# Optimization experiments

Measured on AMD Instinct MI355X. Metric: run time of the kernel, lower is better.

Reference implementation:

```python
import jax, jax.numpy as jnp
import numpy as np

J = 24       # num_joints
DIM = 3      # point dim
CD = 128     # c_dim
BN = 4       # bottleneck_size
HPG = 32     # hidden per group (hidden_size=768 / 24)

def setup_inputs() -> dict:
    key = jax.random.key(0)
    ks = jax.random.split(key, 16)
    B, T = 4, 25000
    s = lambda k, shape, fan_in: jax.random.normal(k, shape, jnp.float32) * (1.0 / np.sqrt(fan_in))
    return {
        "p": jax.random.normal(ks[0], (B, J * DIM, T), jnp.float32),
        "z": jax.random.normal(ks[1], (B, 128), jnp.float32),
        "c": jax.random.normal(ks[2], (B, CD), jnp.float32),
        # grouped Conv1d weights stored as (J, out_per_group, in_per_group)
        "W_proj": s(ks[3], (J, BN, CD), CD),          "b_proj": jnp.zeros((J * BN,), jnp.float32),
        "W_p":   s(ks[4], (J, HPG, DIM + BN), DIM+BN), "b_p":   jnp.zeros((J * HPG,), jnp.float32),
        "W0":    s(ks[5], (J, HPG, HPG), HPG),         "b0":    jnp.zeros((J * HPG,), jnp.float32),
        "W1":    s(ks[6], (J, HPG, HPG), HPG),         "b1":    jnp.zeros((J * HPG,), jnp.float32),
        "W2":    s(ks[7], (J, HPG, HPG), HPG),         "b2":    jnp.zeros((J * HPG,), jnp.float32),
        "W_out": s(ks[8], (J, 1, HPG), HPG),           "b_out": jnp.zeros((J,), jnp.float32),
    }

def _gconv(x, W, b):
    # grouped 1x1 conv: x (B,J,Cin,T), W (J,Cout,Cin), b (J*Cout,) -> (B,J,Cout,T)
    y = jnp.einsum('bjit,joi->bjot', x, W)
    return y + b.reshape(1, J, -1, 1)

def reference(p, z, c, W_proj, b_proj, W_p, b_p, W0, b0, W1, b1, W2, b2, W_out, b_out):
    B, _, T = p.shape
    # p.view(B, J, -1, T) then keep last `dim` channels
    p_in = p.reshape(B, J, -1, T)[:, :, -DIM:, :]            # (B,J,3,T)
    # 2D c branch: repeat per joint, grouped proj, broadcast over T
    c_rep = jnp.broadcast_to(c[:, None, :], (B, J, CD))       # (B,J,128)
    c_proj = jnp.einsum('bjc,joc->bjo', c_rep, W_proj) + b_proj.reshape(1, J, BN)
    c_proj = jnp.broadcast_to(c_proj[:, :, :, None], (B, J, BN, T))
    x = jnp.concatenate([p_in, c_proj], axis=2)               # (B,J,3+4,T)
    net = jax.nn.relu(_gconv(x,   W_p, b_p))
    net = jax.nn.relu(_gconv(net, W0,  b0))
    net = jax.nn.relu(_gconv(net, W1,  b1))
    net = jax.nn.relu(_gconv(net, W2,  b2))
    out = _gconv(net, W_out, b_out)                           # (B,J,1,T)
    return out.reshape(B, J, T)                               # logits (B, num_joints, T)
```

## Files before the change

kernel.cpp:

```cpp
#include <hip/hip_runtime.h>
#include <hip/hip_bf16.h>

#define NJ 24
#define TLEN 25000
#define NB 4
#define CHUNKS 10
#define NWPB (CHUNKS*4)
#define NITERS ((TLEN+63)/64)

typedef short short8 __attribute__((ext_vector_type(8)));
typedef short s16x2 __attribute__((ext_vector_type(2)));
typedef float f32x16 __attribute__((ext_vector_type(16)));

union FragU { unsigned u[4]; short8 s; };

__device__ __forceinline__ unsigned pack2(float a, float b){
    unsigned ua = __float_as_uint(a) + 0x8000u;
    unsigned ub = __float_as_uint(b) + 0x8000u;
    return __builtin_amdgcn_perm(ub, ua, 0x07060302u);
}
__device__ __forceinline__ float bflo(unsigned u){
    union { unsigned v; float f; } t; t.v = u << 16; return t.f;
}
__device__ __forceinline__ float bfhi(unsigned u){
    union { unsigned v; float f; } t; t.v = u & 0xffff0000u; return t.f;
}
__device__ __forceinline__ void split2(float a, float b, unsigned &hi, unsigned &lo){
    unsigned hw = pack2(a, b);
    float fa = bflo(hw), fb = bfhi(hw);
    lo = pack2(a - fa, b - fb);
    hi = hw;
}

__device__ __forceinline__ unsigned pkrelu(unsigned x){
    union { unsigned u; s16x2 v; } a, r;
    a.u = x;
    s16x2 z; z[0] = 0; z[1] = 0;
    r.v = __builtin_elementwise_max(a.v, z);
    return r.u;
}

__device__ __forceinline__ f32x16 mfma(const FragU &a, const FragU &b, f32x16 c){
    return __builtin_amdgcn_mfma_f32_32x32x16_bf16(a.s, b.s, c, 0, 0, 0);
}

__device__ __forceinline__ void relu_pack(const f32x16 &acc, FragU &k0, FragU &k1){
    unsigned w[8];
    #pragma unroll
    for (int i = 0; i < 8; ++i) w[i] = pkrelu(pack2(acc[2*i], acc[2*i+1]));
    k0.u[0]=w[0]; k0.u[1]=w[1]; k0.u[2]=w[2]; k0.u[3]=w[3];
    k1.u[0]=w[4]; k1.u[1]=w[5]; k1.u[2]=w[6]; k1.u[3]=w[7];
}

__global__ __launch_bounds__(256, 2) void ptf_decoder_kernel(
    const float* __restrict__ p,    const float* __restrict__ c,
    const float* __restrict__ Wproj,const float* __restrict__ bproj,
    const float* __restrict__ Wp,   const float* __restrict__ bp,
    const float* __restrict__ W0,   const float* __restrict__ b0,
    const float* __restrict__ W1,   const float* __restrict__ b1,
    const float* __restrict__ W2,   const float* __restrict__ b2,
    const float* __restrict__ Wout, const float* __restrict__ bout,
    float* __restrict__ out)
{
    __shared__ __align__(16) float ldsW[3][32][36];
    __shared__ __align__(16) float ldsWp[32][8];
    __shared__ __align__(16) float ldsB[4][32];
    __shared__ __align__(16) float ldsWo[32];

    const int tid = threadIdx.x;
    const int bj  = blockIdx.x % (NB*NJ);
    const int sub = blockIdx.x / (NB*NJ);
    const int b   = bj / NJ;
    const int j   = bj % NJ;

    {
        const float* Wl[3] = {W0, W1, W2};
        #pragma unroll
        for (int L = 0; L < 3; ++L) {
            int row = tid >> 3, c4 = tid & 7;
            float4 v = *reinterpret_cast<const float4*>(Wl[L] + ((size_t)(j*32 + row))*32 + c4*4);
            *reinterpret_cast<float4*>(&ldsW[L][row][c4*4]) = v;
        }
        {
            int row = tid >> 3, i8 = tid & 7;
            ldsWp[row][i8] = (i8 < 7) ? Wp[((size_t)(j*32 + row))*7 + i8] : 0.f;
        }
        if      (tid < 32)  ldsB[0][tid]      = bp[j*32 + tid];
        else if (tid < 64)  ldsB[1][tid-32]   = b0[j*32 + tid-32];
        else if (tid < 96)  ldsB[2][tid-64]   = b1[j*32 + tid-64];
        else if (tid < 128) ldsB[3][tid-96]   = b2[j*32 + tid-96];
        else if (tid < 160) ldsWo[tid-128]    = Wout[j*32 + tid-128];
    }
    __syncthreads();

    const int lane = tid & 63;
    const int row  = lane & 31;
    const int h    = lane >> 5;

    FragU whi[3][2];
    #pragma unroll
    for (int L = 0; L < 3; ++L) {
        #pragma unroll
        for (int kh = 0; kh < 2; ++kh) {
            const int g  = kh*2 + h;
            const int cA = (g >> 1)*4 + (g & 1);
            const float* base = &ldsW[L][row][0];
            float4 x = *reinterpret_cast<const float4*>(base + cA*4);
            float4 y = *reinterpret_cast<const float4*>(base + (cA+2)*4);
            whi[L][kh].u[0] = pack2(x.x, x.y);
            whi[L][kh].u[1] = pack2(x.z, x.w);
            whi[L][kh].u[2] = pack2(y.x, y.y);
            whi[L][kh].u[3] = pack2(y.z, y.w);
        }
    }
    FragU woF[2];
    #pragma unroll
    for (int kh = 0; kh < 2; ++kh) {
        const int g  = kh*2 + h;
        const int cA = (g >> 1)*4 + (g & 1);
        float4 x = *reinterpret_cast<const float4*>(&ldsWo[cA*4]);
        float4 y = *reinterpret_cast<const float4*>(&ldsWo[(cA+2)*4]);
        woF[kh].u[0] = pack2(x.x, x.y);
        woF[kh].u[1] = pack2(x.z, x.w);
        woF[kh].u[2] = pack2(y.x, y.y);
        woF[kh].u[3] = pack2(y.z, y.w);
    }
    FragU wphi, wplo;
    {
        float4 x = make_float4(0,0,0,0), y = make_float4(0,0,0,0);
        if (lane < 32) {
            x = *reinterpret_cast<const float4*>(&ldsWp[row][0]);
            y = *reinterpret_cast<const float4*>(&ldsWp[row][4]);
        }
        split2(x.x, x.y, wphi.u[0], wplo.u[0]);
        split2(x.z, x.w, wphi.u[1], wplo.u[1]);
        split2(y.x, y.y, wphi.u[2], wplo.u[2]);
        split2(y.z, y.w, wphi.u[3], wplo.u[3]);
    }

    f32x16 biasP, biasL0, biasL1, biasL2;
    #pragma unroll
    for (int q = 0; q < 4; ++q) {
        float4 v0 = *reinterpret_cast<const float4*>(&ldsB[0][q*8 + 4*h]);
        float4 v1 = *reinterpret_cast<const float4*>(&ldsB[1][q*8 + 4*h]);
        float4 v2 = *reinterpret_cast<const float4*>(&ldsB[2][q*8 + 4*h]);
        float4 v3 = *reinterpret_cast<const float4*>(&ldsB[3][q*8 + 4*h]);
        biasP[q*4+0]=v0.x; biasP[q*4+1]=v0.y; biasP[q*4+2]=v0.z; biasP[q*4+3]=v0.w;
        biasL0[q*4+0]=v1.x; biasL0[q*4+1]=v1.y; biasL0[q*4+2]=v1.z; biasL0[q*4+3]=v1.w;
        biasL1[q*4+0]=v2.x; biasL1[q*4+1]=v2.y; biasL1[q*4+2]=v2.z; biasL1[q*4+3]=v2.w;
        biasL2[q*4+0]=v3.x; biasL2[q*4+1]=v3.y; biasL2[q*4+2]=v3.z; biasL2[q*4+3]=v3.w;
    }
    const float bo = bout[j];
    f32x16 biasOut;
    #pragma unroll
    for (int r = 0; r < 16; ++r) biasOut[r] = bo;

    float cacc0, cacc1, cacc2, cacc3;
    {
        const float* cb  = c + (size_t)b*128;
        const float* wpj = Wproj + (size_t)j*4*128;
        float cl = cb[lane], chv = cb[lane + 64];
        cacc0 = cl*wpj[0*128+lane] + chv*wpj[0*128+lane+64];
        cacc1 = cl*wpj[1*128+lane] + chv*wpj[1*128+lane+64];
        cacc2 = cl*wpj[2*128+lane] + chv*wpj[2*128+lane+64];
        cacc3 = cl*wpj[3*128+lane] + chv*wpj[3*128+lane+64];
        #pragma unroll
        for (int off = 32; off >= 1; off >>= 1) {
            cacc0 += __shfl_xor(cacc0, off, 64);
            cacc1 += __shfl_xor(cacc1, off, 64);
            cacc2 += __shfl_xor(cacc2, off, 64);
            cacc3 += __shfl_xor(cacc3, off, 64);
        }
        cacc0 += bproj[j*4+0]; cacc1 += bproj[j*4+1];
        cacc2 += bproj[j*4+2]; cacc3 += bproj[j*4+3];
    }
    const float c0v = (lane < 32) ? cacc0 : 0.f;
    unsigned wc2h = pack2(cacc1, cacc2);
    unsigned wc3h = pack2(cacc3, 0.f);
    if (lane >= 32) { wc2h = 0; wc3h = 0; }

    const float* pb0 = p + ((size_t)(b*(NJ*3) + j*3 + 0))*TLEN;
    const float* pb1 = pb0 + TLEN;
    const float* pb2 = pb1 + TLEN;
    float* ob = out + ((size_t)(b*NJ + j))*TLEN;

    const int w0idx = sub*4 + (tid >> 6);

    auto loadP = [&](int itx, float&x0,float&x1,float&x2,float&x3,float&x4,float&x5){
        x0=0.f;x1=0.f;x2=0.f;x3=0.f;x4=0.f;x5=0.f;
        if (itx < NITERS && lane < 32) {
            int tA = itx*64 + lane;
            int tB = tA + 32;
            tA = tA < TLEN ? tA : TLEN-1;
            tB = tB < TLEN ? tB : TLEN-1;
            x0 = pb0[tA]; x1 = pb1[tA]; x2 = pb2[tA];
            x3 = pb0[tB]; x4 = pb1[tB]; x5 = pb2[tB];
        }
    };

    float a0,a1,a2,a3,a4,a5;
    loadP(w0idx, a0,a1,a2,a3,a4,a5);

    for (int it = w0idx; it < NITERS; it += NWPB) {
        float n0,n1,n2,n3,n4,n5;
        loadP(it + NWPB, n0,n1,n2,n3,n4,n5);

        FragU fAh, fBh;
        fAh.u[0] = pack2(a0, a1);  fAh.u[1] = pack2(a2, c0v);
        fBh.u[0] = pack2(a3, a4);  fBh.u[1] = pack2(a5, c0v);
        fAh.u[2]=wc2h; fAh.u[3]=wc3h;
        fBh.u[2]=wc2h; fBh.u[3]=wc3h;

        f32x16 accA, accB;
        accA = mfma(wphi, fAh, biasP);
        accB = mfma(wphi, fBh, biasP);
        accA = mfma(wplo, fAh, accA);
        accB = mfma(wplo, fBh, accB);

        #pragma unroll
        for (int L = 0; L < 3; ++L) {
            FragU pA0, pA1, pB0, pB1;
            relu_pack(accA, pA0, pA1);
            relu_pack(accB, pB0, pB1);
            const f32x16 bb = (L==0) ? biasL0 : (L==1) ? biasL1 : biasL2;
            accA = mfma(whi[L][0], pA0, bb);
            accB = mfma(whi[L][0], pB0, bb);
            accA = mfma(whi[L][1], pA1, accA);
            accB = mfma(whi[L][1], pB1, accB);
        }

        FragU qA0, qA1, qB0, qB1;
        relu_pack(accA, qA0, qA1);
        relu_pack(accB, qB0, qB1);
        f32x16 oA = mfma(woF[0], qA0, biasOut);
        f32x16 oB = mfma(woF[0], qB0, biasOut);
        oA = mfma(woF[1], qA1, oA);
        oB = mfma(woF[1], qB1, oB);

        int t = it*64 + lane;
        if (t < TLEN) ob[t] = (lane < 32) ? oA[0] : oB[0];

        a0=n0; a1=n1; a2=n2; a3=n3; a4=n4; a5=n5;
    }
}

extern "C" void kernel_launch(void* const* d_in, const int* in_sizes, int n_in,
                              void* d_out, int out_size, void* d_ws, size_t ws_size,
                              hipStream_t stream) {
    const float* p     = (const float*)d_in[0];
    const float* c     = (const float*)d_in[2];
    const float* Wproj = (const float*)d_in[3];
    const float* bproj = (const float*)d_in[4];
    const float* Wp    = (const float*)d_in[5];
    const float* bp    = (const float*)d_in[6];
    const float* W0    = (const float*)d_in[7];
    const float* b0    = (const float*)d_in[8];
    const float* W1    = (const float*)d_in[9];
    const float* b1    = (const float*)d_in[10];
    const float* W2    = (const float*)d_in[11];
    const float* b2    = (const float*)d_in[12];
    const float* Wout  = (const float*)d_in[13];
    const float* bout  = (const float*)d_in[14];
    float* out = (float*)d_out;

    dim3 grid(NB*NJ*CHUNKS), block(256);
    ptf_decoder_kernel<<<grid, block, 0, stream>>>(
        p, c, Wproj, bproj, Wp, bp, W0, b0, W1, b1, W2, b2, Wout, bout, out);
}
```

Before: 38.55 us.

## Fold biases into MFMA operands to free bias accumulator registers

The first-layer bias is folded into the input projection as an extra weight column multiplied by a constant-one input channel. Hidden-layer biases are rebuilt each iteration by a small rank-1 MFMA from packed hi/lo bf16 bias values times ones, and the output bias is added as a scalar at the store. This drops four 16-float bias accumulators held in registers, lowering VGPR pressure, at the cost of three extra MFMAs per iteration.

```diff
diff --git a/kernel.cpp b/kernel.cpp
--- a/kernel.cpp
+++ b/kernel.cpp
@@ -42,6 +42,10 @@
 
 __device__ __forceinline__ f32x16 mfma(const FragU &a, const FragU &b, f32x16 c){
     return __builtin_amdgcn_mfma_f32_32x32x16_bf16(a.s, b.s, c, 0, 0, 0);
+}
+
+__device__ __forceinline__ FragU mk1(unsigned w){
+    FragU f; f.u[0] = w; f.u[1] = 0; f.u[2] = 0; f.u[3] = 0; return f;
 }
 
 __device__ __forceinline__ void relu_pack(const f32x16 &acc, FragU &k0, FragU &k1){
@@ -64,7 +68,7 @@
 {
     __shared__ __align__(16) float ldsW[3][32][36];
     __shared__ __align__(16) float ldsWp[32][8];
-    __shared__ __align__(16) float ldsB[4][32];
+    __shared__ __align__(16) float ldsB[3][32];
     __shared__ __align__(16) float ldsWo[32];
 
     const int tid = threadIdx.x;
@@ -83,13 +87,13 @@
         }
         {
             int row = tid >> 3, i8 = tid & 7;
-            ldsWp[row][i8] = (i8 < 7) ? Wp[((size_t)(j*32 + row))*7 + i8] : 0.f;
-        }
-        if      (tid < 32)  ldsB[0][tid]      = bp[j*32 + tid];
-        else if (tid < 64)  ldsB[1][tid-32]   = b0[j*32 + tid-32];
-        else if (tid < 96)  ldsB[2][tid-64]   = b1[j*32 + tid-64];
-        else if (tid < 128) ldsB[3][tid-96]   = b2[j*32 + tid-96];
-        else if (tid < 160) ldsWo[tid-128]    = Wout[j*32 + tid-128];
+            ldsWp[row][i8] = (i8 < 7) ? Wp[((size_t)(j*32 + row))*7 + i8]
+                                      : bp[j*32 + row];
+        }
+        if      (tid < 32)  ldsB[0][tid]      = b0[j*32 + tid];
+        else if (tid < 64)  ldsB[1][tid-32]   = b1[j*32 + tid-32];
+        else if (tid < 96)  ldsB[2][tid-64]   = b2[j*32 + tid-64];
+        else if (tid < 128) ldsWo[tid-96]     = Wout[j*32 + tid-96];
     }
     __syncthreads();
 
@@ -138,22 +142,19 @@
         split2(y.z, y.w, wphi.u[3], wplo.u[3]);
     }
 
-    f32x16 biasP, biasL0, biasL1, biasL2;
-    #pragma unroll
-    for (int q = 0; q < 4; ++q) {
-        float4 v0 = *reinterpret_cast<const float4*>(&ldsB[0][q*8 + 4*h]);
-        float4 v1 = *reinterpret_cast<const float4*>(&ldsB[1][q*8 + 4*h]);
-        float4 v2 = *reinterpret_cast<const float4*>(&ldsB[2][q*8 + 4*h]);
-        float4 v3 = *reinterpret_cast<const float4*>(&ldsB[3][q*8 + 4*h]);
-        biasP[q*4+0]=v0.x; biasP[q*4+1]=v0.y; biasP[q*4+2]=v0.z; biasP[q*4+3]=v0.w;
-        biasL0[q*4+0]=v1.x; biasL0[q*4+1]=v1.y; biasL0[q*4+2]=v1.z; biasL0[q*4+3]=v1.w;
-        biasL1[q*4+0]=v2.x; biasL1[q*4+1]=v2.y; biasL1[q*4+2]=v2.z; biasL1[q*4+3]=v2.w;
-        biasL2[q*4+0]=v3.x; biasL2[q*4+1]=v3.y; biasL2[q*4+2]=v3.z; biasL2[q*4+3]=v3.w;
-    }
-    const float bo = bout[j];
-    f32x16 biasOut;
-    #pragma unroll
-    for (int r = 0; r < 16; ++r) biasOut[r] = bo;
+    unsigned biasA[3];
+    #pragma unroll
+    for (int L = 0; L < 3; ++L) {
+        float bl = (h == 0) ? ldsB[L][row] : 0.f;
+        unsigned t = pack2(bl, 0.f);
+        float res = bl - bflo(t);
+        biasA[L] = (h == 0) ? pack2(bl, res) : 0u;
+    }
+    const unsigned ones2 = (h == 0) ? 0x3f803f80u : 0u;
+
+    f32x16 kZero;
+    #pragma unroll
+    for (int r = 0; r < 16; ++r) kZero[r] = 0.f;
 
     float cacc0, cacc1, cacc2, cacc3;
     {
@@ -176,8 +177,9 @@
     }
     const float c0v = (lane < 32) ? cacc0 : 0.f;
     unsigned wc2h = pack2(cacc1, cacc2);
-    unsigned wc3h = pack2(cacc3, 0.f);
+    unsigned wc3h = pack2(cacc3, 1.0f);
     if (lane >= 32) { wc2h = 0; wc3h = 0; }
+    const float bo = bout[j];
 
     const float* pb0 = p + ((size_t)(b*(NJ*3) + j*3 + 0))*TLEN;
     const float* pb1 = pb0 + TLEN;
@@ -212,19 +214,19 @@
         fBh.u[2]=wc2h; fBh.u[3]=wc3h;
 
         f32x16 accA, accB;
-        accA = mfma(wphi, fAh, biasP);
-        accB = mfma(wphi, fBh, biasP);
+        accA = mfma(wphi, fAh, kZero);
+        accB = mfma(wphi, fBh, kZero);
         accA = mfma(wplo, fAh, accA);
         accB = mfma(wplo, fBh, accB);
 
         #pragma unroll
         for (int L = 0; L < 3; ++L) {
+            f32x16 bAcc = mfma(mk1(biasA[L]), mk1(ones2), kZero);
             FragU pA0, pA1, pB0, pB1;
             relu_pack(accA, pA0, pA1);
             relu_pack(accB, pB0, pB1);
-            const f32x16 bb = (L==0) ? biasL0 : (L==1) ? biasL1 : biasL2;
-            accA = mfma(whi[L][0], pA0, bb);
-            accB = mfma(whi[L][0], pB0, bb);
+            accA = mfma(whi[L][0], pA0, bAcc);
+            accB = mfma(whi[L][0], pB0, bAcc);
             accA = mfma(whi[L][1], pA1, accA);
             accB = mfma(whi[L][1], pB1, accB);
         }
@@ -232,13 +234,13 @@
         FragU qA0, qA1, qB0, qB1;
         relu_pack(accA, qA0, qA1);
         relu_pack(accB, qB0, qB1);
-        f32x16 oA = mfma(woF[0], qA0, biasOut);
-        f32x16 oB = mfma(woF[0], qB0, biasOut);
+        f32x16 oA = mfma(woF[0], qA0, kZero);
+        f32x16 oB = mfma(woF[0], qB0, kZero);
         oA = mfma(woF[1], qA1, oA);
         oB = mfma(woF[1], qB1, oB);
 
         int t = it*64 + lane;
-        if (t < TLEN) ob[t] = (lane < 32) ? oA[0] : oB[0];
+        if (t < TLEN) ob[t] = ((lane < 32) ? oA[0] : oB[0]) + bo;
 
         a0=n0; a1=n1; a2=n2; a3=n3; a4=n4; a5=n5;
     }
```

After: 36.01 us. -6.6%, faster.
